# Performance work log

Hardware: AMD Instinct MI355X
Metric: run time of the kernel (lower is better)

## Reference

```python
import jax, jax.numpy as jnp
import numpy as np

EPS = 1e-6
BETA = 0.25
COMMIT_W = 1.0


def setup_inputs() -> dict:
    key = jax.random.key(0)
    k1, k2, k3 = jax.random.split(key, 3)
    b, c, h, w = 8, 256, 32, 32
    n_e, e_dim = 16384, 256
    z = jax.random.normal(k1, (b, c, h, w), jnp.float32)
    # frozen_codebook = randn(n_e, e_dim) * e_dim**-0.5
    codebook = jax.random.normal(k2, (n_e, e_dim), jnp.float32) * (e_dim ** -0.5)
    # nn.Linear(e_dim, in_channels, bias=False) weight: (in_channels, e_dim)
    W = jax.random.normal(k3, (c, e_dim), jnp.float32) * (e_dim ** -0.5)
    return {"z": z, "codebook": codebook, "W": W}


def _rotate_to(src, tgt):
    # Rotation trick (Fifty et al.): rotate src onto tgt direction with a
    # detached Householder-style transform; gradient flows through src only.
    # src, tgt: (n, d)
    norm_src = jnp.linalg.norm(src, axis=-1, keepdims=True)
    norm_tgt = jnp.linalg.norm(tgt, axis=-1, keepdims=True)
    u = src / (norm_src + EPS)
    q = tgt / (norm_tgt + EPS)
    uq = u + q
    w_ = jax.lax.stop_gradient(uq / (jnp.linalg.norm(uq, axis=-1, keepdims=True) + EPS))
    u_d = jax.lax.stop_gradient(u)
    q_d = jax.lax.stop_gradient(q)
    rot = (src
           - 2.0 * jnp.sum(src * w_, axis=-1, keepdims=True) * w_
           + 2.0 * jnp.sum(src * u_d, axis=-1, keepdims=True) * q_d)
    return rot * jax.lax.stop_gradient(norm_tgt / (norm_src + EPS))


def reference(z, codebook, W):
    b, c, h, w = z.shape
    # b c h w -> (b*h*w, c)
    z_flat = jnp.transpose(z, (0, 2, 3, 1)).reshape(-1, c)
    # implicit codebook: frozen codes through linear projection
    emb = codebook @ W.T  # (n_e, c)
    # squared L2 distances (no grad needed for argmin)
    d = (jnp.sum(z_flat ** 2, axis=1, keepdims=True)
         + jnp.sum(emb ** 2, axis=1)
         - 2.0 * (z_flat @ emb.T))  # (n_tok, n_e)
    indices = jnp.argmin(d, axis=1)  # (n_tok,)
    z_q_flat = emb[indices]  # gather quantized vectors
    loss = COMMIT_W * (jnp.mean((jax.lax.stop_gradient(z_flat) - z_q_flat) ** 2)
                       + BETA * jnp.mean((z_flat - jax.lax.stop_gradient(z_q_flat)) ** 2))
    z_q_flat = _rotate_to(z_flat, z_q_flat)
    z_q = jnp.transpose(z_q_flat.reshape(b, h, w, c), (0, 3, 1, 2))
    return z_q, loss, indices
```

## Files before the change

### kernel.cpp

```cpp
#include <hip/hip_runtime.h>
#include <math.h>

#define EPSV 1e-6f
#define NTOK 8192
#define NE   16384
#define DIM  256

using short8 = __attribute__((ext_vector_type(8))) short;
using f32x4v = __attribute__((ext_vector_type(4))) float;

__device__ __forceinline__ unsigned short f2bf(float v) {
    unsigned int u = __float_as_uint(v);
    u += 0x7fffu + ((u >> 16) & 1u);
    return (unsigned short)(u >> 16);
}
__device__ __forceinline__ float bf2f(unsigned short h) {
    return __uint_as_float(((unsigned int)h) << 16);
}

__device__ __forceinline__ void gload_lds16(const void* g, void* s) {
    __builtin_amdgcn_global_load_lds(
        (const __attribute__((address_space(1))) void*)g,
        (__attribute__((address_space(3))) void*)s, 16, 0, 0);
}

__device__ __forceinline__ void split8(const float4 a, const float4 b,
                                       short8& h, short8& l) {
    float f[8] = {a.x, a.y, a.z, a.w, b.x, b.y, b.z, b.w};
#pragma unroll
    for (int j = 0; j < 8; ++j) {
        unsigned short hh = f2bf(f[j]);
        h[j] = (short)hh;
        l[j] = (short)f2bf(f[j] - bf2f(hh));
    }
}

__global__ __launch_bounds__(256) void f1_pre(
    const float* __restrict__ zin, float* __restrict__ z_flat,
    unsigned short* __restrict__ zh, unsigned short* __restrict__ zl,
    float* __restrict__ sz, const float* __restrict__ Wm,
    unsigned short* __restrict__ wh, unsigned short* __restrict__ wl) {
    const int bid = blockIdx.x;
    const int tid = threadIdx.x;
    if (bid >= 128) {
        const int i = ((bid - 128) * 256 + tid) * 4;
        const float4 v = *(const float4*)(Wm + i);
        float f[4] = {v.x, v.y, v.z, v.w};
#pragma unroll
        for (int j = 0; j < 4; ++j) {
            unsigned short h = f2bf(f[j]);
            wh[i + j] = h;
            wl[i + j] = f2bf(f[j] - bf2f(h));
        }
        return;
    }
    __shared__ float tile[64][65];
    const int yx0 = (bid & 15) * 64, b = bid >> 4;
    const int sub = tid >> 6, ln = tid & 63;
    double dacc[16];
#pragma unroll
    for (int j = 0; j < 16; ++j) dacc[j] = 0.0;

    for (int cc = 0; cc < 4; ++cc) {
        const int c0 = cc * 64;
        __syncthreads();
#pragma unroll
        for (int j = 0; j < 16; ++j) {
            int cl = j * 4 + sub;
            tile[cl][ln] = zin[((size_t)(b * 256 + c0 + cl) << 10) + yx0 + ln];
        }
        __syncthreads();
#pragma unroll
        for (int j = 0; j < 16; ++j) {
            int tl = j * 4 + sub;
            float v = tile[ln][tl];
            size_t o = (size_t)(b * 1024 + yx0 + tl) * 256 + c0 + ln;
            z_flat[o] = v;
            unsigned short h = f2bf(v);
            zh[o] = h;
            zl[o] = f2bf(v - bf2f(h));
            dacc[j] += (double)v * v;
        }
    }
#pragma unroll
    for (int j = 0; j < 16; ++j) {
        double s = dacc[j];
#pragma unroll
        for (int m = 1; m < 64; m <<= 1) s += __shfl_xor(s, m);
        if (ln == 0) sz[b * 1024 + yx0 + j * 4 + sub] = (float)s;
    }
}

__global__ __launch_bounds__(256, 2) void k0c_emb(
    const float* __restrict__ cb, const unsigned short* __restrict__ wh,
    const unsigned short* __restrict__ wl, float* __restrict__ emb,
    unsigned short* __restrict__ eh, unsigned short* __restrict__ el,
    float* __restrict__ se0, float* __restrict__ se1) {
    __shared__ char smemC[65536];
    const int tid = threadIdx.x;
    const int w = tid >> 6, lane = tid & 63;
    const int quad = lane >> 4, lr = lane & 15;
    const int wr = w & 1, wc = w >> 1;
    const int n0 = blockIdx.x * 128, c0 = blockIdx.y * 128;

    f32x4v acc[4][4];
#pragma unroll
    for (int mt = 0; mt < 4; ++mt)
#pragma unroll
        for (int nt = 0; nt < 4; ++nt)
            acc[mt][nt] = (f32x4v){0.f, 0.f, 0.f, 0.f};

    for (int kc = 0; kc < 4; ++kc) {
        __syncthreads();
#pragma unroll
        for (int i = 0; i < 16; ++i) {
            int s = i * 4 + w;
            int u = s * 64 + lane;
            const void* g;
            if (s < 32) {
                int kg = u >> 7, row = u & 127;
                g = cb + (size_t)(n0 + row) * 256 + kc * 64 + kg * 4;
            } else if (s < 48) {
                int u1 = u - 2048;
                int kg = u1 >> 7, row = u1 & 127;
                g = wh + (size_t)(c0 + row) * 256 + kc * 64 + kg * 8;
            } else {
                int u2 = u - 3072;
                int kg = u2 >> 7, row = u2 & 127;
                g = wl + (size_t)(c0 + row) * 256 + kc * 64 + kg * 8;
            }
            gload_lds16(g, smemC + ((size_t)u << 4));
        }
        __syncthreads();
#pragma unroll
        for (int ks = 0; ks < 2; ++ks) {
            short8 Ah[4], Al[4], Bh[4], Bl[4];
#pragma unroll
            for (int mt = 0; mt < 4; ++mt) {
                int m = wr * 64 + mt * 16 + lr;
                int kg2 = ks * 8 + quad * 2;
                float4 f0 = *(const float4*)(smemC + (((size_t)kg2 * 128 + m) << 4));
                float4 f1 = *(const float4*)(smemC + ((((size_t)kg2 + 1) * 128 + m) << 4));
                split8(f0, f1, Ah[mt], Al[mt]);
            }
#pragma unroll
            for (int nt = 0; nt < 4; ++nt) {
                int n = wc * 64 + nt * 16 + lr;
                int ku = (ks * 4 + quad) * 128 + n;
                Bh[nt] = *(const short8*)(smemC + (((size_t)2048 + ku) << 4));
                Bl[nt] = *(const short8*)(smemC + (((size_t)3072 + ku) << 4));
            }
#pragma unroll
            for (int mt = 0; mt < 4; ++mt)
#pragma unroll
                for (int nt = 0; nt < 4; ++nt) {
                    f32x4v a = acc[mt][nt];
                    a = __builtin_amdgcn_mfma_f32_16x16x32_bf16(Ah[mt], Bh[nt], a, 0, 0, 0);
                    a = __builtin_amdgcn_mfma_f32_16x16x32_bf16(Ah[mt], Bl[nt], a, 0, 0, 0);
                    a = __builtin_amdgcn_mfma_f32_16x16x32_bf16(Al[mt], Bh[nt], a, 0, 0, 0);
                    a = __builtin_amdgcn_mfma_f32_16x16x32_bf16(Al[mt], Bl[nt], a, 0, 0, 0);
                    acc[mt][nt] = a;
                }
        }
    }
#pragma unroll
    for (int mt = 0; mt < 4; ++mt)
#pragma unroll
        for (int rr = 0; rr < 4; ++rr) {
            int row = n0 + wr * 64 + mt * 16 + quad * 4 + rr;
#pragma unroll
            for (int nt = 0; nt < 4; ++nt) {
                int col = c0 + wc * 64 + nt * 16 + lr;
                size_t o = (size_t)row * 256 + col;
                float v = acc[mt][nt][rr];
                emb[o] = v;
                unsigned short h = f2bf(v);
                eh[o] = h;
                el[o] = f2bf(v - bf2f(h));
            }
        }
    __syncthreads();
    float* sblk = (float*)smemC;
#pragma unroll
    for (int mt = 0; mt < 4; ++mt)
#pragma unroll
        for (int rr = 0; rr < 4; ++rr) {
            float s = 0.f;
#pragma unroll
            for (int nt = 0; nt < 4; ++nt) {
                float v = acc[mt][nt][rr];
                s = fmaf(v, v, s);
            }
#pragma unroll
            for (int st = 1; st < 16; st <<= 1) s += __shfl_xor(s, st);
            if (lr == 0)
                sblk[wc * 128 + wr * 64 + mt * 16 + quad * 4 + rr] = s;
        }
    __syncthreads();
    if (tid < 128) {
        float* sep = (blockIdx.y == 0) ? se0 : se1;
        sep[n0 + tid] = sblk[tid] + sblk[128 + tid];
    }
}

__global__ __launch_bounds__(256, 2) void k1_dist_argmin(
    const unsigned short* __restrict__ zh, const unsigned short* __restrict__ zl,
    const unsigned short* __restrict__ eh, const unsigned short* __restrict__ el,
    const float* __restrict__ sz, const float* __restrict__ se0,
    const float* __restrict__ se1, float* __restrict__ pval,
    int* __restrict__ pidx) {
    __shared__ short8 smem[2][2048];
    const int tid = threadIdx.x;
    const int w = tid >> 6, lane = tid & 63;
    const int quad = lane >> 4, lr = lane & 15;
    const int tokBase = blockIdx.x * 128;
    const int rowBase = tokBase + w * 32;
    const int slab = blockIdx.y;
    const int slabBase = slab * 2048;

    short8 Ah[2][8], Al[2][8];
#pragma unroll
    for (int mt = 0; mt < 2; ++mt)
#pragma unroll
        for (int ks = 0; ks < 8; ++ks) {
            size_t o = (size_t)(rowBase + mt * 16 + lr) * 256 + ks * 32 + quad * 8;
            Ah[mt][ks] = *(const short8*)(zh + o);
            Al[mt][ks] = *(const short8*)(zl + o);
        }

    float szr[2][4];
#pragma unroll
    for (int mt = 0; mt < 2; ++mt)
#pragma unroll
        for (int rr = 0; rr < 4; ++rr)
            szr[mt][rr] = sz[rowBase + mt * 16 + quad * 4 + rr];

    float minv[2][4];
    int mini[2][4];
#pragma unroll
    for (int mt = 0; mt < 2; ++mt)
#pragma unroll
        for (int rr = 0; rr < 4; ++rr) {
            minv[mt][rr] = INFINITY;
            mini[mt][rr] = 0;
        }

    auto stage = [&](int buf, int ch) {
        const int colBase = slabBase + ch * 32;
#pragma unroll
        for (int i = 0; i < 8; ++i) {
            int u = i * 256 + tid;
            int fmt = u >> 10;
            int u1 = u & 1023;
            int col = u1 >> 5, kgs = u1 & 31;
            int kg = kgs ^ col;
            const unsigned short* g =
                (fmt ? el : eh) + (size_t)(colBase + col) * 256 + kg * 8;
            gload_lds16(g, (char*)&smem[0][0] + buf * 32768 +
                               (((size_t)i * 256 + w * 64) << 4));
        }
    };

    stage(0, 0);
    __syncthreads();

    for (int ch = 0; ch < 64; ++ch) {
        const int cur = ch & 1;
        if (ch + 1 < 64) stage(cur ^ 1, ch + 1);

        const int colg0 = slabBase + ch * 32 + lr;
        const int colg1 = colg0 + 16;
        const float sec0 = se0[colg0] + se1[colg0];
        const float sec1 = se0[colg1] + se1[colg1];

        f32x4v acc[2][2];
#pragma unroll
        for (int mt = 0; mt < 2; ++mt)
#pragma unroll
            for (int nt = 0; nt < 2; ++nt)
                acc[mt][nt] = (f32x4v){0.f, 0.f, 0.f, 0.f};

#pragma unroll
        for (int ks = 0; ks < 8; ++ks) {
            short8 Bh[2], Bl[2];
#pragma unroll
            for (int nt = 0; nt < 2; ++nt) {
                int col = nt * 16 + lr;
                int kgs = (ks * 4 + quad) ^ col;
                Bh[nt] = smem[cur][col * 32 + kgs];
                Bl[nt] = smem[cur][1024 + col * 32 + kgs];
            }
#pragma unroll
            for (int mt = 0; mt < 2; ++mt)
#pragma unroll
                for (int nt = 0; nt < 2; ++nt) {
                    f32x4v a = acc[mt][nt];
                    a = __builtin_amdgcn_mfma_f32_16x16x32_bf16(Ah[mt][ks], Bh[nt], a, 0, 0, 0);
                    a = __builtin_amdgcn_mfma_f32_16x16x32_bf16(Ah[mt][ks], Bl[nt], a, 0, 0, 0);
                    a = __builtin_amdgcn_mfma_f32_16x16x32_bf16(Al[mt][ks], Bh[nt], a, 0, 0, 0);
                    acc[mt][nt] = a;
                }
        }

        const int colBase = slabBase + ch * 32;
#pragma unroll
        for (int nt = 0; nt < 2; ++nt) {
            const int colg = colBase + nt * 16 + lr;
            const float sec = nt ? sec1 : sec0;
#pragma unroll
            for (int mt = 0; mt < 2; ++mt)
#pragma unroll
                for (int rr = 0; rr < 4; ++rr) {
                    float szse = __fadd_rn(szr[mt][rr], sec);
                    float d = fmaf(-2.0f, acc[mt][nt][rr], szse);
                    if (d < minv[mt][rr]) {
                        minv[mt][rr] = d;
                        mini[mt][rr] = colg;
                    }
                }
        }
        __syncthreads();
    }

#pragma unroll
    for (int st = 1; st < 16; st <<= 1) {
#pragma unroll
        for (int mt = 0; mt < 2; ++mt)
#pragma unroll
            for (int rr = 0; rr < 4; ++rr) {
                float ov = __shfl_xor(minv[mt][rr], st);
                int oi = __shfl_xor(mini[mt][rr], st);
                if (ov < minv[mt][rr] ||
                    (ov == minv[mt][rr] && oi < mini[mt][rr])) {
                    minv[mt][rr] = ov;
                    mini[mt][rr] = oi;
                }
            }
    }
    if (lr == 0) {
#pragma unroll
        for (int mt = 0; mt < 2; ++mt)
#pragma unroll
            for (int rr = 0; rr < 4; ++rr) {
                int row = rowBase + mt * 16 + quad * 4 + rr;
                pval[(size_t)row * 8 + slab] = minv[mt][rr];
                pidx[(size_t)row * 8 + slab] = mini[mt][rr];
            }
    }
}

__global__ __launch_bounds__(256) void k3a_token(
    const float* __restrict__ z_flat, const float* __restrict__ emb,
    const float* __restrict__ pval, const int* __restrict__ pidx,
    float* __restrict__ alpha, float* __restrict__ beta,
    int* __restrict__ idxf, float* __restrict__ out,
    float* __restrict__ lpart) {
    __shared__ float red[4];
    const int w = threadIdx.x >> 6, lane = threadIdx.x & 63;
    const int t = blockIdx.x * 4 + w;

    float bv = INFINITY;
    int bi = 0x7fffffff;
    if (lane < 8) {
        bv = pval[(size_t)t * 8 + lane];
        bi = pidx[(size_t)t * 8 + lane];
    }
#pragma unroll
    for (int st = 1; st < 8; st <<= 1) {
        float ov = __shfl_xor(bv, st);
        int oi = __shfl_xor(bi, st);
        if (ov < bv || (ov == bv && oi < bi)) { bv = ov; bi = oi; }
    }
    const int best = __shfl(bi, 0);

    const float4 zv = *(const float4*)(z_flat + (size_t)t * 256 + lane * 4);
    const float4 ev = *(const float4*)(emb + (size_t)best * 256 + lane * 4);
    float szs = zv.x * zv.x + zv.y * zv.y + zv.z * zv.z + zv.w * zv.w;
    float ses = ev.x * ev.x + ev.y * ev.y + ev.z * ev.z + ev.w * ev.w;
    float zes = zv.x * ev.x + zv.y * ev.y + zv.z * ev.z + zv.w * ev.w;
    float dx = zv.x - ev.x, dy = zv.y - ev.y, dz = zv.z - ev.z, dw = zv.w - ev.w;
    float sqs = dx * dx + dy * dy + dz * dz + dw * dw;
#pragma unroll
    for (int m = 1; m < 64; m <<= 1) {
        szs += __shfl_xor(szs, m);
        ses += __shfl_xor(ses, m);
        zes += __shfl_xor(zes, m);
        sqs += __shfl_xor(sqs, m);
    }
    if (lane == 0) {
        float ns = sqrtf(szs), nt = sqrtf(ses);
        float inv_s = 1.0f / (ns + EPSV);
        float inv_t = 1.0f / (nt + EPSV);
        float s2 = szs * inv_s;
        float su = szs * inv_s * inv_s;
        float sq = ses * inv_t * inv_t;
        float uq = zes * inv_s * inv_t;
        float nw = sqrtf(su + sq + 2.0f * uq);
        float inv_w = 1.0f / (nw + EPSV);
        float s1 = (s2 + zes * inv_t) * inv_w;
        float scale = nt * inv_s;
        float a = scale * (1.0f - 2.0f * s1 * inv_w * inv_s);
        float bb = scale * inv_t * 2.0f * (s2 - s1 * inv_w);
        alpha[t] = a;
        beta[t] = bb;
        idxf[t] = best;
        out[2097153 + t] = (float)best;
        red[w] = sqs;
    }
    __syncthreads();
    if (threadIdx.x == 0)
        lpart[blockIdx.x] = red[0] + red[1] + red[2] + red[3];
}

__global__ __launch_bounds__(256) void k3b_zq(
    const float* __restrict__ zin, const float* __restrict__ emb,
    const float* __restrict__ alpha, const float* __restrict__ beta,
    const int* __restrict__ idxf, const float* __restrict__ lpart,
    float* __restrict__ out) {
    if (blockIdx.x == 0) {
        __shared__ float red[4];
        const int tid = threadIdx.x;
        float s = 0.0f;
        for (int i = tid; i < 2048; i += 256) s += lpart[i];
#pragma unroll
        for (int m = 1; m < 64; m <<= 1) s += __shfl_xor(s, m);
        if ((tid & 63) == 0) red[tid >> 6] = s;
        __syncthreads();
        if (tid == 0)
            out[2097152] = 1.25f * (red[0] + red[1] + red[2] + red[3]) *
                           (1.0f / 2097152.0f);
    }
    const int i = blockIdx.x * 256 + threadIdx.x;
    const int c = (i >> 10) & 255;
    const int t = ((i >> 18) << 10) | (i & 1023);
    out[i] = alpha[t] * zin[i] + beta[t] * emb[(size_t)idxf[t] * 256 + c];
}

extern "C" void kernel_launch(void* const* d_in, const int* in_sizes, int n_in,
                              void* d_out, int out_size, void* d_ws,
                              size_t ws_size, hipStream_t stream) {
    (void)in_sizes; (void)n_in; (void)out_size; (void)ws_size;
    const float* zin = (const float*)d_in[0];
    const float* cb  = (const float*)d_in[1];
    const float* Wm  = (const float*)d_in[2];
    float* out = (float*)d_out;
    char* ws = (char*)d_ws;

    float*          z_flat = (float*)(ws + 0);
    unsigned short* zh     = (unsigned short*)(ws + 8388608);
    unsigned short* zl     = (unsigned short*)(ws + 12582912);
    float*          emb    = (float*)(ws + 16777216);
    unsigned short* eh     = (unsigned short*)(ws + 33554432);
    unsigned short* el     = (unsigned short*)(ws + 41943040);
    float*          sz     = (float*)(ws + 50331648);
    float*          se0    = (float*)(ws + 50364416);
    float*          se1    = (float*)(ws + 50429952);
    float*          pval   = (float*)(ws + 50495488);
    int*            pidx   = (int*)(ws + 50757632);
    float*          alpha  = (float*)(ws + 51019776);
    float*          beta   = (float*)(ws + 51052544);
    int*            idxf   = (int*)(ws + 51085312);
    float*          lpart  = (float*)(ws + 51118080);
    unsigned short* wh     = (unsigned short*)(ws + 51126272);
    unsigned short* wl     = (unsigned short*)(ws + 51257344);

    f1_pre<<<192, 256, 0, stream>>>(zin, z_flat, zh, zl, sz, Wm, wh, wl);
    k0c_emb<<<dim3(128, 2), 256, 0, stream>>>(cb, wh, wl, emb, eh, el,
                                              se0, se1);
    k1_dist_argmin<<<dim3(64, 8), 256, 0, stream>>>(zh, zl, eh, el, sz,
                                                    se0, se1, pval, pidx);
    k3a_token<<<2048, 256, 0, stream>>>(z_flat, emb, pval, pidx, alpha, beta,
                                        idxf, out, lpart);
    k3b_zq<<<8192, 256, 0, stream>>>(zin, emb, alpha, beta, idxf, lpart, out);
}
```

Before: 284.0 us.

## Software-pipeline distance epilogue with next chunk's MFMA using ping-pong accumulators

Restructures the chunk loop so the argmin epilogue for chunk ch-1 runs after issuing the MFMAs for chunk ch, using two accumulator sets and a manually unrolled-by-two loop. The codebook-norm loads for the next chunk are also fetched ahead. The aim is to hide the compare/select epilogue latency behind matrix-core work. In exchange it doubles accumulator registers, which may reduce occupancy.

New measurement: 498.1 us. +75.4%, slower.

```diff
diff --git a/kernel.cpp b/kernel.cpp
--- a/kernel.cpp
+++ b/kernel.cpp
@@ -261,25 +261,12 @@
         }
     };
 
-    stage(0, 0);
-    __syncthreads();
-
-    for (int ch = 0; ch < 64; ++ch) {
-        const int cur = ch & 1;
-        if (ch + 1 < 64) stage(cur ^ 1, ch + 1);
-
-        const int colg0 = slabBase + ch * 32 + lr;
-        const int colg1 = colg0 + 16;
-        const float sec0 = se0[colg0] + se1[colg0];
-        const float sec1 = se0[colg1] + se1[colg1];
-
-        f32x4v acc[2][2];
+    auto compute = [&](f32x4v (&acc)[2][2], int cur) {
 #pragma unroll
         for (int mt = 0; mt < 2; ++mt)
 #pragma unroll
             for (int nt = 0; nt < 2; ++nt)
                 acc[mt][nt] = (f32x4v){0.f, 0.f, 0.f, 0.f};
-
 #pragma unroll
         for (int ks = 0; ks < 8; ++ks) {
             short8 Bh[2], Bl[2];
@@ -301,12 +288,14 @@
                     acc[mt][nt] = a;
                 }
         }
-
-        const int colBase = slabBase + ch * 32;
+    };
+
+    auto epilogue = [&](const f32x4v (&acc)[2][2], float s0, float s1,
+                        int colBase) {
 #pragma unroll
         for (int nt = 0; nt < 2; ++nt) {
             const int colg = colBase + nt * 16 + lr;
-            const float sec = nt ? sec1 : sec0;
+            const float sec = nt ? s1 : s0;
 #pragma unroll
             for (int mt = 0; mt < 2; ++mt)
 #pragma unroll
@@ -319,8 +308,52 @@
                     }
                 }
         }
-        __syncthreads();
-    }
+    };
+
+    f32x4v accA[2][2], accB[2][2];
+
+    stage(0, 0);
+    __syncthreads();
+
+    stage(1, 1);
+    float psec0 = se0[slabBase + lr] + se1[slabBase + lr];
+    float psec1 = se0[slabBase + 16 + lr] + se1[slabBase + 16 + lr];
+    int pcol = slabBase;
+    compute(accA, 0);
+    __syncthreads();
+
+#pragma unroll 1
+    for (int ch = 1; ch < 63; ch += 2) {
+        stage(0, ch + 1);
+        {
+            const int cb0 = slabBase + ch * 32;
+            float c0 = se0[cb0 + lr] + se1[cb0 + lr];
+            float c1 = se0[cb0 + 16 + lr] + se1[cb0 + 16 + lr];
+            compute(accB, 1);
+            epilogue(accA, psec0, psec1, pcol);
+            psec0 = c0; psec1 = c1; pcol = cb0;
+        }
+        __syncthreads();
+        stage(1, ch + 2);
+        {
+            const int cb0 = slabBase + (ch + 1) * 32;
+            float c0 = se0[cb0 + lr] + se1[cb0 + lr];
+            float c1 = se0[cb0 + 16 + lr] + se1[cb0 + 16 + lr];
+            compute(accA, 0);
+            epilogue(accB, psec0, psec1, pcol);
+            psec0 = c0; psec1 = c1; pcol = cb0;
+        }
+        __syncthreads();
+    }
+    {
+        const int cb0 = slabBase + 63 * 32;
+        float c0 = se0[cb0 + lr] + se1[cb0 + lr];
+        float c1 = se0[cb0 + 16 + lr] + se1[cb0 + 16 + lr];
+        compute(accB, 1);
+        epilogue(accA, psec0, psec1, pcol);
+        psec0 = c0; psec1 = c1; pcol = cb0;
+    }
+    epilogue(accB, psec0, psec1, pcol);
 
 #pragma unroll
     for (int st = 1; st < 16; st <<= 1) {
```

## Shrink distance-argmin tile to 16x16 per wave for more blocks and occupancy

Applied to the files above, without the earlier changes.

The distance/argmin kernel's per-wave tile drops from 32 tokens x 32 codes to 16 tokens x 16 codes. Block count rises from 512 to 1024 with a flattened grid where consecutive blocks share token rows across slabs, and occupancy is raised to 4 blocks per CU with half the LDS. The aim is better CU fill and latency hiding. In exchange each staged codebook chunk feeds half as many MFMAs, so LDS/global traffic per FLOP doubles, and there are twice as many barriers per block.

After: 301.6 us. 6.2% more time.

```diff
diff --git a/kernel.cpp b/kernel.cpp
--- a/kernel.cpp
+++ b/kernel.cpp
@@ -203,60 +203,54 @@
     }
 }
 
-__global__ __launch_bounds__(256, 2) void k1_dist_argmin(
+__global__ __launch_bounds__(256, 4) void k1_dist_argmin(
     const unsigned short* __restrict__ zh, const unsigned short* __restrict__ zl,
     const unsigned short* __restrict__ eh, const unsigned short* __restrict__ el,
     const float* __restrict__ sz, const float* __restrict__ se0,
     const float* __restrict__ se1, float* __restrict__ pval,
     int* __restrict__ pidx) {
-    __shared__ short8 smem[2][2048];
+    __shared__ short8 smem[2][1024];
     const int tid = threadIdx.x;
     const int w = tid >> 6, lane = tid & 63;
     const int quad = lane >> 4, lr = lane & 15;
-    const int tokBase = blockIdx.x * 128;
-    const int rowBase = tokBase + w * 32;
-    const int slab = blockIdx.y;
+    const int bid = blockIdx.x;
+    const int slab = bid & 7;
+    const int rowBase = (bid >> 3) * 64 + w * 16;
     const int slabBase = slab * 2048;
 
-    short8 Ah[2][8], Al[2][8];
-#pragma unroll
-    for (int mt = 0; mt < 2; ++mt)
-#pragma unroll
-        for (int ks = 0; ks < 8; ++ks) {
-            size_t o = (size_t)(rowBase + mt * 16 + lr) * 256 + ks * 32 + quad * 8;
-            Ah[mt][ks] = *(const short8*)(zh + o);
-            Al[mt][ks] = *(const short8*)(zl + o);
-        }
-
-    float szr[2][4];
-#pragma unroll
-    for (int mt = 0; mt < 2; ++mt)
-#pragma unroll
-        for (int rr = 0; rr < 4; ++rr)
-            szr[mt][rr] = sz[rowBase + mt * 16 + quad * 4 + rr];
-
-    float minv[2][4];
-    int mini[2][4];
-#pragma unroll
-    for (int mt = 0; mt < 2; ++mt)
-#pragma unroll
-        for (int rr = 0; rr < 4; ++rr) {
-            minv[mt][rr] = INFINITY;
-            mini[mt][rr] = 0;
-        }
+    short8 Ah[8], Al[8];
+#pragma unroll
+    for (int ks = 0; ks < 8; ++ks) {
+        size_t o = (size_t)(rowBase + lr) * 256 + ks * 32 + quad * 8;
+        Ah[ks] = *(const short8*)(zh + o);
+        Al[ks] = *(const short8*)(zl + o);
+    }
+
+    float szr[4];
+#pragma unroll
+    for (int rr = 0; rr < 4; ++rr)
+        szr[rr] = sz[rowBase + quad * 4 + rr];
+
+    float minv[4];
+    int mini[4];
+#pragma unroll
+    for (int rr = 0; rr < 4; ++rr) {
+        minv[rr] = INFINITY;
+        mini[rr] = 0;
+    }
 
     auto stage = [&](int buf, int ch) {
-        const int colBase = slabBase + ch * 32;
-#pragma unroll
-        for (int i = 0; i < 8; ++i) {
+        const int colBase = slabBase + ch * 16;
+#pragma unroll
+        for (int i = 0; i < 4; ++i) {
             int u = i * 256 + tid;
-            int fmt = u >> 10;
-            int u1 = u & 1023;
+            int fmt = u >> 9;
+            int u1 = u & 511;
             int col = u1 >> 5, kgs = u1 & 31;
             int kg = kgs ^ col;
             const unsigned short* g =
                 (fmt ? el : eh) + (size_t)(colBase + col) * 256 + kg * 8;
-            gload_lds16(g, (char*)&smem[0][0] + buf * 32768 +
+            gload_lds16(g, (char*)&smem[0][0] + buf * 16384 +
                                (((size_t)i * 256 + w * 64) << 4));
         }
     };
@@ -264,60 +258,33 @@
     stage(0, 0);
     __syncthreads();
 
-    for (int ch = 0; ch < 64; ++ch) {
+    for (int ch = 0; ch < 128; ++ch) {
         const int cur = ch & 1;
-        if (ch + 1 < 64) stage(cur ^ 1, ch + 1);
-
-        const int colg0 = slabBase + ch * 32 + lr;
-        const int colg1 = colg0 + 16;
-        const float sec0 = se0[colg0] + se1[colg0];
-        const float sec1 = se0[colg1] + se1[colg1];
-
-        f32x4v acc[2][2];
-#pragma unroll
-        for (int mt = 0; mt < 2; ++mt)
-#pragma unroll
-            for (int nt = 0; nt < 2; ++nt)
-                acc[mt][nt] = (f32x4v){0.f, 0.f, 0.f, 0.f};
+        if (ch + 1 < 128) stage(cur ^ 1, ch + 1);
+
+        const int colg = slabBase + ch * 16 + lr;
+        const float sec = se0[colg] + se1[colg];
+
+        f32x4v acc = (f32x4v){0.f, 0.f, 0.f, 0.f};
 
 #pragma unroll
         for (int ks = 0; ks < 8; ++ks) {
-            short8 Bh[2], Bl[2];
-#pragma unroll
-            for (int nt = 0; nt < 2; ++nt) {
-                int col = nt * 16 + lr;
-                int kgs = (ks * 4 + quad) ^ col;
-                Bh[nt] = smem[cur][col * 32 + kgs];
-                Bl[nt] = smem[cur][1024 + col * 32 + kgs];
-            }
-#pragma unroll
-            for (int mt = 0; mt < 2; ++mt)
-#pragma unroll
-                for (int nt = 0; nt < 2; ++nt) {
-                    f32x4v a = acc[mt][nt];
-                    a = __builtin_amdgcn_mfma_f32_16x16x32_bf16(Ah[mt][ks], Bh[nt], a, 0, 0, 0);
-                    a = __builtin_amdgcn_mfma_f32_16x16x32_bf16(Ah[mt][ks], Bl[nt], a, 0, 0, 0);
-                    a = __builtin_amdgcn_mfma_f32_16x16x32_bf16(Al[mt][ks], Bh[nt], a, 0, 0, 0);
-                    acc[mt][nt] = a;
-                }
-        }
-
-        const int colBase = slabBase + ch * 32;
-#pragma unroll
-        for (int nt = 0; nt < 2; ++nt) {
-            const int colg = colBase + nt * 16 + lr;
-            const float sec = nt ? sec1 : sec0;
-#pragma unroll
-            for (int mt = 0; mt < 2; ++mt)
-#pragma unroll
-                for (int rr = 0; rr < 4; ++rr) {
-                    float szse = __fadd_rn(szr[mt][rr], sec);
-                    float d = fmaf(-2.0f, acc[mt][nt][rr], szse);
-                    if (d < minv[mt][rr]) {
-                        minv[mt][rr] = d;
-                        mini[mt][rr] = colg;
-                    }
-                }
+            const int kgs = (ks * 4 + quad) ^ lr;
+            short8 Bh = smem[cur][lr * 32 + kgs];
+            short8 Bl = smem[cur][512 + lr * 32 + kgs];
+            acc = __builtin_amdgcn_mfma_f32_16x16x32_bf16(Ah[ks], Bh, acc, 0, 0, 0);
+            acc = __builtin_amdgcn_mfma_f32_16x16x32_bf16(Ah[ks], Bl, acc, 0, 0, 0);
+            acc = __builtin_amdgcn_mfma_f32_16x16x32_bf16(Al[ks], Bh, acc, 0, 0, 0);
+        }
+
+#pragma unroll
+        for (int rr = 0; rr < 4; ++rr) {
+            float szse = __fadd_rn(szr[rr], sec);
+            float d = fmaf(-2.0f, acc[rr], szse);
+            if (d < minv[rr]) {
+                minv[rr] = d;
+                mini[rr] = colg;
+            }
         }
         __syncthreads();
     }
@@ -325,27 +292,23 @@
 #pragma unroll
     for (int st = 1; st < 16; st <<= 1) {
 #pragma unroll
-        for (int mt = 0; mt < 2; ++mt)
-#pragma unroll
-            for (int rr = 0; rr < 4; ++rr) {
-                float ov = __shfl_xor(minv[mt][rr], st);
-                int oi = __shfl_xor(mini[mt][rr], st);
-                if (ov < minv[mt][rr] ||
-                    (ov == minv[mt][rr] && oi < mini[mt][rr])) {
-                    minv[mt][rr] = ov;
-                    mini[mt][rr] = oi;
-                }
-            }
+        for (int rr = 0; rr < 4; ++rr) {
+            float ov = __shfl_xor(minv[rr], st);
+            int oi = __shfl_xor(mini[rr], st);
+            if (ov < minv[rr] ||
+                (ov == minv[rr] && oi < mini[rr])) {
+                minv[rr] = ov;
+                mini[rr] = oi;
+            }
+        }
     }
     if (lr == 0) {
 #pragma unroll
-        for (int mt = 0; mt < 2; ++mt)
-#pragma unroll
-            for (int rr = 0; rr < 4; ++rr) {
-                int row = rowBase + mt * 16 + quad * 4 + rr;
-                pval[(size_t)row * 8 + slab] = minv[mt][rr];
-                pidx[(size_t)row * 8 + slab] = mini[mt][rr];
-            }
+        for (int rr = 0; rr < 4; ++rr) {
+            int row = rowBase + quad * 4 + rr;
+            pval[(size_t)row * 8 + slab] = minv[rr];
+            pidx[(size_t)row * 8 + slab] = mini[rr];
+        }
     }
 }
 
@@ -467,8 +430,8 @@
     f1_pre<<<192, 256, 0, stream>>>(zin, z_flat, zh, zl, sz, Wm, wh, wl);
     k0c_emb<<<dim3(128, 2), 256, 0, stream>>>(cb, wh, wl, emb, eh, el,
                                               se0, se1);
-    k1_dist_argmin<<<dim3(64, 8), 256, 0, stream>>>(zh, zl, eh, el, sz,
-                                                    se0, se1, pval, pidx);
+    k1_dist_argmin<<<1024, 256, 0, stream>>>(zh, zl, eh, el, sz,
+                                             se0, se1, pval, pidx);
     k3a_token<<<2048, 256, 0, stream>>>(z_flat, emb, pval, pidx, alpha, beta,
                                         idxf, out, lpart);
     k3b_zq<<<8192, 256, 0, stream>>>(zin, emb, alpha, beta, idxf, lpart, out);
```

## Fuse z transpose into emb kernel, cache codebook norms in LDS, vectorize output

Applied to the files above, without the earlier changes.

Splits the W bf16 split into its own small kernel and merges the z transpose/split blocks into the embedding GEMM kernel, so both run in one launch over a 1D grid. The distance kernel now preloads the summed codebook squared norms for its slab into shared memory once instead of reading two global arrays every chunk, and its grid is remapped so consecutive blocks share token rows. The final output kernel processes four elements per thread with float4 loads and stores. The cost is extra LDS use in the argmin kernel, which could lower occupancy.

Measured after the change: 283.8 us. About the same (-0.1%).

```diff
diff --git a/kernel.cpp b/kernel.cpp
--- a/kernel.cpp
+++ b/kernel.cpp
@@ -35,73 +35,78 @@
     }
 }
 
-__global__ __launch_bounds__(256) void f1_pre(
-    const float* __restrict__ zin, float* __restrict__ z_flat,
-    unsigned short* __restrict__ zh, unsigned short* __restrict__ zl,
-    float* __restrict__ sz, const float* __restrict__ Wm,
-    unsigned short* __restrict__ wh, unsigned short* __restrict__ wl) {
-    const int bid = blockIdx.x;
-    const int tid = threadIdx.x;
-    if (bid >= 128) {
-        const int i = ((bid - 128) * 256 + tid) * 4;
-        const float4 v = *(const float4*)(Wm + i);
-        float f[4] = {v.x, v.y, v.z, v.w};
-#pragma unroll
-        for (int j = 0; j < 4; ++j) {
-            unsigned short h = f2bf(f[j]);
-            wh[i + j] = h;
-            wl[i + j] = f2bf(f[j] - bf2f(h));
-        }
-        return;
-    }
-    __shared__ float tile[64][65];
-    const int yx0 = (bid & 15) * 64, b = bid >> 4;
-    const int sub = tid >> 6, ln = tid & 63;
-    double dacc[16];
-#pragma unroll
-    for (int j = 0; j < 16; ++j) dacc[j] = 0.0;
-
-    for (int cc = 0; cc < 4; ++cc) {
-        const int c0 = cc * 64;
-        __syncthreads();
-#pragma unroll
-        for (int j = 0; j < 16; ++j) {
-            int cl = j * 4 + sub;
-            tile[cl][ln] = zin[((size_t)(b * 256 + c0 + cl) << 10) + yx0 + ln];
-        }
-        __syncthreads();
-#pragma unroll
-        for (int j = 0; j < 16; ++j) {
-            int tl = j * 4 + sub;
-            float v = tile[ln][tl];
-            size_t o = (size_t)(b * 1024 + yx0 + tl) * 256 + c0 + ln;
-            z_flat[o] = v;
-            unsigned short h = f2bf(v);
-            zh[o] = h;
-            zl[o] = f2bf(v - bf2f(h));
-            dacc[j] += (double)v * v;
-        }
-    }
-#pragma unroll
-    for (int j = 0; j < 16; ++j) {
-        double s = dacc[j];
-#pragma unroll
-        for (int m = 1; m < 64; m <<= 1) s += __shfl_xor(s, m);
-        if (ln == 0) sz[b * 1024 + yx0 + j * 4 + sub] = (float)s;
-    }
-}
-
-__global__ __launch_bounds__(256, 2) void k0c_emb(
+__global__ __launch_bounds__(256) void fW_pre(
+    const float* __restrict__ Wm, unsigned short* __restrict__ wh,
+    unsigned short* __restrict__ wl) {
+    const int i = (blockIdx.x * 256 + threadIdx.x) * 4;
+    const float4 v = *(const float4*)(Wm + i);
+    float f[4] = {v.x, v.y, v.z, v.w};
+#pragma unroll
+    for (int j = 0; j < 4; ++j) {
+        unsigned short h = f2bf(f[j]);
+        wh[i + j] = h;
+        wl[i + j] = f2bf(f[j] - bf2f(h));
+    }
+}
+
+__global__ __launch_bounds__(256, 2) void k0c_fz(
     const float* __restrict__ cb, const unsigned short* __restrict__ wh,
     const unsigned short* __restrict__ wl, float* __restrict__ emb,
     unsigned short* __restrict__ eh, unsigned short* __restrict__ el,
-    float* __restrict__ se0, float* __restrict__ se1) {
-    __shared__ char smemC[65536];
+    float* __restrict__ se0, float* __restrict__ se1,
+    const float* __restrict__ zin, float* __restrict__ z_flat,
+    unsigned short* __restrict__ zh, unsigned short* __restrict__ zl,
+    float* __restrict__ sz) {
+    __shared__ char smemU[65536];
+    const int bid = blockIdx.x;
     const int tid = threadIdx.x;
+
+    if (bid >= 256) {
+        float (*tile)[65] = (float(*)[65])smemU;
+        const int zbid = bid - 256;
+        const int yx0 = (zbid & 15) * 64, b = zbid >> 4;
+        const int sub = tid >> 6, ln = tid & 63;
+        double dacc[16];
+#pragma unroll
+        for (int j = 0; j < 16; ++j) dacc[j] = 0.0;
+
+        for (int cc = 0; cc < 4; ++cc) {
+            const int c0 = cc * 64;
+            __syncthreads();
+#pragma unroll
+            for (int j = 0; j < 16; ++j) {
+                int cl = j * 4 + sub;
+                tile[cl][ln] = zin[((size_t)(b * 256 + c0 + cl) << 10) + yx0 + ln];
+            }
+            __syncthreads();
+#pragma unroll
+            for (int j = 0; j < 16; ++j) {
+                int tl = j * 4 + sub;
+                float v = tile[ln][tl];
+                size_t o = (size_t)(b * 1024 + yx0 + tl) * 256 + c0 + ln;
+                z_flat[o] = v;
+                unsigned short h = f2bf(v);
+                zh[o] = h;
+                zl[o] = f2bf(v - bf2f(h));
+                dacc[j] += (double)v * v;
+            }
+        }
+#pragma unroll
+        for (int j = 0; j < 16; ++j) {
+            double s = dacc[j];
+#pragma unroll
+            for (int m = 1; m < 64; m <<= 1) s += __shfl_xor(s, m);
+            if (ln == 0) sz[b * 1024 + yx0 + j * 4 + sub] = (float)s;
+        }
+        return;
+    }
+
+    char* smemC = smemU;
     const int w = tid >> 6, lane = tid & 63;
     const int quad = lane >> 4, lr = lane & 15;
     const int wr = w & 1, wc = w >> 1;
-    const int n0 = blockIdx.x * 128, c0 = blockIdx.y * 128;
+    const int nb = bid & 127, cbi = bid >> 7;
+    const int n0 = nb * 128, c0 = cbi * 128;
 
     f32x4v acc[4][4];
 #pragma unroll
@@ -198,7 +203,7 @@
         }
     __syncthreads();
     if (tid < 128) {
-        float* sep = (blockIdx.y == 0) ? se0 : se1;
+        float* sep = (cbi == 0) ? se0 : se1;
         sep[n0 + tid] = sblk[tid] + sblk[128 + tid];
     }
 }
@@ -210,13 +215,18 @@
     const float* __restrict__ se1, float* __restrict__ pval,
     int* __restrict__ pidx) {
     __shared__ short8 smem[2][2048];
+    __shared__ float seS[2048];
     const int tid = threadIdx.x;
     const int w = tid >> 6, lane = tid & 63;
     const int quad = lane >> 4, lr = lane & 15;
-    const int tokBase = blockIdx.x * 128;
+    const int bid = blockIdx.x;
+    const int slab = bid & 7;
+    const int tokBase = (bid >> 3) * 128;
     const int rowBase = tokBase + w * 32;
-    const int slab = blockIdx.y;
     const int slabBase = slab * 2048;
+
+    for (int j = tid; j < 2048; j += 256)
+        seS[j] = __fadd_rn(se0[slabBase + j], se1[slabBase + j]);
 
     short8 Ah[2][8], Al[2][8];
 #pragma unroll
@@ -268,10 +278,8 @@
         const int cur = ch & 1;
         if (ch + 1 < 64) stage(cur ^ 1, ch + 1);
 
-        const int colg0 = slabBase + ch * 32 + lr;
-        const int colg1 = colg0 + 16;
-        const float sec0 = se0[colg0] + se1[colg0];
-        const float sec1 = se0[colg1] + se1[colg1];
+        const float sec0 = seS[ch * 32 + lr];
+        const float sec1 = seS[ch * 32 + 16 + lr];
 
         f32x4v acc[2][2];
 #pragma unroll
@@ -430,10 +438,19 @@
             out[2097152] = 1.25f * (red[0] + red[1] + red[2] + red[3]) *
                            (1.0f / 2097152.0f);
     }
-    const int i = blockIdx.x * 256 + threadIdx.x;
-    const int c = (i >> 10) & 255;
-    const int t = ((i >> 18) << 10) | (i & 1023);
-    out[i] = alpha[t] * zin[i] + beta[t] * emb[(size_t)idxf[t] * 256 + c];
+    const int i4 = (blockIdx.x * 256 + threadIdx.x) * 4;
+    const int c = (i4 >> 10) & 255;
+    const int t0 = ((i4 >> 18) << 10) | (i4 & 1023);
+    const float4 zv = *(const float4*)(zin + i4);
+    const float4 av = *(const float4*)(alpha + t0);
+    const float4 bv = *(const float4*)(beta + t0);
+    const int4  iv = *(const int4*)(idxf + t0);
+    float4 o;
+    o.x = av.x * zv.x + bv.x * emb[(size_t)iv.x * 256 + c];
+    o.y = av.y * zv.y + bv.y * emb[(size_t)iv.y * 256 + c];
+    o.z = av.z * zv.z + bv.z * emb[(size_t)iv.z * 256 + c];
+    o.w = av.w * zv.w + bv.w * emb[(size_t)iv.w * 256 + c];
+    *(float4*)(out + i4) = o;
 }
 
 extern "C" void kernel_launch(void* const* d_in, const int* in_sizes, int n_in,
@@ -464,12 +481,12 @@
     unsigned short* wh     = (unsigned short*)(ws + 51126272);
     unsigned short* wl     = (unsigned short*)(ws + 51257344);
 
-    f1_pre<<<192, 256, 0, stream>>>(zin, z_flat, zh, zl, sz, Wm, wh, wl);
-    k0c_emb<<<dim3(128, 2), 256, 0, stream>>>(cb, wh, wl, emb, eh, el,
-                                              se0, se1);
-    k1_dist_argmin<<<dim3(64, 8), 256, 0, stream>>>(zh, zl, eh, el, sz,
-                                                    se0, se1, pval, pidx);
+    fW_pre<<<64, 256, 0, stream>>>(Wm, wh, wl);
+    k0c_fz<<<384, 256, 0, stream>>>(cb, wh, wl, emb, eh, el, se0, se1,
+                                    zin, z_flat, zh, zl, sz);
+    k1_dist_argmin<<<512, 256, 0, stream>>>(zh, zl, eh, el, sz,
+                                            se0, se1, pval, pidx);
     k3a_token<<<2048, 256, 0, stream>>>(z_flat, emb, pval, pidx, alpha, beta,
                                         idxf, out, lpart);
-    k3b_zq<<<8192, 256, 0, stream>>>(zin, emb, alpha, beta, idxf, lpart, out);
-}
+    k3b_zq<<<2048, 256, 0, stream>>>(zin, emb, alpha, beta, idxf, lpart, out);
+}
```
